# Kernel optimization log

Measured on AMD Instinct MI355X. Metric: run time of the kernel, lower is better.

## Reference

```python
import jax, jax.numpy as jnp
import numpy as np
import math

B, T, C, H, S_CACHE = 2, 1024, 2048, 16, 1024
DK = C // H


def setup_inputs() -> dict:
    key = jax.random.key(0)
    ks = jax.random.split(key, 7)
    x = jax.random.normal(ks[0], (B, T, C), dtype=jnp.float32)
    cache_k = jax.random.normal(ks[1], (B, H, S_CACHE, DK), dtype=jnp.float32)
    cache_v = jax.random.normal(ks[2], (B, H, S_CACHE, DK), dtype=jnp.float32)
    scale = 0.02
    Wq = jax.random.normal(ks[3], (C, C), dtype=jnp.float32) * scale
    Wk = jax.random.normal(ks[4], (C, C), dtype=jnp.float32) * scale
    Wv = jax.random.normal(ks[5], (C, C), dtype=jnp.float32) * scale
    Wo = jax.random.normal(ks[6], (C, C), dtype=jnp.float32) * scale
    return {"x": x, "cache_k": cache_k, "cache_v": cache_v,
            "Wq": Wq, "Wk": Wk, "Wv": Wv, "Wo": Wo}


def reference(x, cache_k, cache_v, Wq, Wk, Wv, Wo):
    b, t, c = x.shape
    h = cache_k.shape[1]
    dk = c // h
    # nn.Linear: y = x @ W.T  (weights stored [out, in])
    Q = (x @ Wq.T).reshape(b, t, h, dk).transpose(0, 2, 1, 3)  # [B,H,T,dk]
    K = (x @ Wk.T).reshape(b, t, h, dk).transpose(0, 2, 1, 3)
    V = (x @ Wv.T).reshape(b, t, h, dk).transpose(0, 2, 1, 3)
    K = jnp.concatenate([cache_k, K], axis=2)  # [B,H,S,dk]
    V = jnp.concatenate([cache_v, V], axis=2)
    s = K.shape[2]
    scores = jnp.einsum('bhtd,bhsd->bhts', Q, K) / math.sqrt(dk)
    # faithful to the source: mask = tril(ones(T, S)) (no cache offset); T==1 -> all ones
    if t == 1:
        mask = jnp.ones((1, s), dtype=jnp.float32)
    else:
        mask = jnp.tril(jnp.ones((t, s), dtype=jnp.float32))
    scores = jnp.where(mask == 0, jnp.float32(-jnp.inf), scores)
    attn = jax.nn.softmax(scores, axis=-1)
    out = jnp.einsum('bhts,bhsd->bhtd', attn, V)
    out = out.transpose(0, 2, 1, 3).reshape(b, t, c)
    return (out @ Wo.T, K, V)
```

## Files before the change

### kernel.cpp

```cpp
#include <hip/hip_runtime.h>

typedef unsigned short u16;
typedef short bf16x8 __attribute__((ext_vector_type(8)));
typedef float f32x4 __attribute__((ext_vector_type(4)));
typedef unsigned short u16x4 __attribute__((ext_vector_type(4)));

#define AS1 __attribute__((address_space(1)))
#define AS3 __attribute__((address_space(3)))

__device__ __forceinline__ u16 f2bf(float f) {
    unsigned u = __float_as_uint(f);
    u += 0x7fff + ((u >> 16) & 1);
    return (u16)(u >> 16);
}

__device__ __forceinline__ void gld16(const void* g, void* l) {
    __builtin_amdgcn_global_load_lds((const AS1 void*)g, (AS3 void*)l, 16, 0, 0);
}

__global__ void convall_kernel(const float* __restrict__ x,  const float* __restrict__ wq,
                               const float* __restrict__ wk, const float* __restrict__ wv,
                               const float* __restrict__ wo,
                               u16* __restrict__ xb, u16* __restrict__ wqkv, u16* __restrict__ wob) {
    int t = blockIdx.x * 256 + threadIdx.x;
    const float* srcs[5] = { x, wq, wk, wv, wo };
    u16* dsts[5] = { xb, wqkv, wqkv + 4194304, wqkv + 8388608, wob };
#pragma unroll
    for (int r = 0; r < 5; r++) {
        f32x4 v = ((const f32x4*)srcs[r])[t];
        u16x4 o = { f2bf(v.x), f2bf(v.y), f2bf(v.z), f2bf(v.w) };
        ((u16x4*)dsts[r])[t] = o;
    }
}

__global__ void cachek_kernel(const float* __restrict__ ck, float* __restrict__ kout,
                              u16* __restrict__ kcb) {
    const int n4 = (2 * 16 * 1024 * 128) / 4;
    int i = blockIdx.x * 256 + threadIdx.x;
    int stride = gridDim.x * 256;
    for (; i < n4; i += stride) {
        f32x4 v = ((const f32x4*)ck)[i];
        int bh = i >> 15;
        ((f32x4*)kout)[i + bh * 32768] = v;
        u16x4 o = { f2bf(v.x), f2bf(v.y), f2bf(v.z), f2bf(v.w) };
        ((u16x4*)kcb)[i] = o;
    }
}

__global__ void vtrans_kernel(const float* __restrict__ cv, float* __restrict__ vout,
                              u16* __restrict__ vtb) {
    __shared__ u16 tile[64 * 65];
    const int bh = blockIdx.x;
    const int s0 = blockIdx.y * 64;
    const int d0 = blockIdx.z * 64;
    const float* src = cv + (size_t)bh * 1024 * 128;
#pragma unroll
    for (int i = 0; i < 16; i++) {
        int e = i * 256 + threadIdx.x;
        int sr = e >> 6, dc = e & 63;
        float v = src[(size_t)(s0 + sr) * 128 + d0 + dc];
        vout[((size_t)bh * 2048 + s0 + sr) * 128 + d0 + dc] = v;
        tile[sr * 65 + dc] = f2bf(v);
    }
    __syncthreads();
    u16* dst = vtb + (size_t)bh * 128 * 1024;
#pragma unroll
    for (int i = 0; i < 16; i++) {
        int e = i * 256 + threadIdx.x;
        int dr = e >> 6, sc = e & 63;
        dst[(size_t)(d0 + dr) * 1024 + s0 + sc] = tile[sc * 65 + dr];
    }
}

template <int MODE>
__global__ __launch_bounds__(256) void gemm_bt_kernel(
    const u16* __restrict__ A, const u16* __restrict__ Bm,
    u16* __restrict__ qout, float* __restrict__ kout, float* __restrict__ vout,
    float* __restrict__ cout) {
    __shared__ u16 As[128 * 64];
    __shared__ u16 Bs[128 * 64];
    const int tid = threadIdx.x;
    const int lane = tid & 63, wv = tid >> 6;
    const int wm = (wv >> 1) * 64, wn = (wv & 1) * 64;
    const int m0 = blockIdx.y * 128, n0 = blockIdx.x * 128;
    const int frow = lane & 15, fq = lane >> 4;
    const int swz = frow & 7;

    f32x4 acc[4][4];
#pragma unroll
    for (int a = 0; a < 4; a++)
#pragma unroll
        for (int b = 0; b < 4; b++) acc[a][b] = (f32x4){0.f, 0.f, 0.f, 0.f};

    for (int k0 = 0; k0 < 2048; k0 += 64) {
        __syncthreads();
#pragma unroll
        for (int i = 0; i < 4; i++) {
            int L = i * 256 + tid;
            int row = L >> 3;
            int c = (L & 7) ^ (row & 7);
            gld16(A + (size_t)(m0 + row) * 2048 + k0 + c * 8, As + i * 2048 + wv * 512);
            gld16(Bm + (size_t)(n0 + row) * 2048 + k0 + c * 8, Bs + i * 2048 + wv * 512);
        }
        __syncthreads();
#pragma unroll
        for (int kk = 0; kk < 2; kk++) {
            bf16x8 aF[4], bF[4];
#pragma unroll
            for (int f = 0; f < 4; f++) {
                aF[f] = *(const bf16x8*)(As + (wm + f * 16 + frow) * 64 + ((kk * 4 + fq) ^ swz) * 8);
                bF[f] = *(const bf16x8*)(Bs + (wn + f * 16 + frow) * 64 + ((kk * 4 + fq) ^ swz) * 8);
            }
#pragma unroll
            for (int fm = 0; fm < 4; fm++)
#pragma unroll
                for (int fn = 0; fn < 4; fn++)
                    acc[fm][fn] = __builtin_amdgcn_mfma_f32_16x16x32_bf16(aF[fm], bF[fn], acc[fm][fn], 0, 0, 0);
        }
    }

#pragma unroll
    for (int fm = 0; fm < 4; fm++) {
#pragma unroll
        for (int fn = 0; fn < 4; fn++) {
#pragma unroll
            for (int r = 0; r < 4; r++) {
                int m = m0 + wm + fm * 16 + fq * 4 + r;
                int n = n0 + wn + fn * 16 + frow;
                float v = acc[fm][fn][r];
                if (MODE == 0) {
                    int b = m >> 10, t = m & 1023;
                    int sect = n >> 11, nn = n & 2047;
                    int h = nn >> 7, d = nn & 127;
                    size_t bh = (size_t)(b * 16 + h);
                    if (sect == 0)
                        qout[(bh * 1024 + t) * 128 + d] = f2bf(v * 0.08838834764831843f);
                    else if (sect == 1)
                        kout[(bh * 2048 + 1024 + t) * 128 + d] = v;
                    else
                        vout[(bh * 2048 + 1024 + t) * 128 + d] = v;
                } else {
                    cout[(size_t)m * 2048 + n] = v;
                }
            }
        }
    }
}

__global__ __launch_bounds__(256) void attn_kernel(
    const u16* __restrict__ Qb, const u16* __restrict__ Kcb,
    const u16* __restrict__ Vtb, u16* __restrict__ AOb) {
    __shared__ u16 Qs[64 * 128];
    __shared__ u16 Ks[64 * 128];
    __shared__ u16 Vs[128 * 64];
    __shared__ u16 Ps[64 * 64];
    int bid = blockIdx.x;
    int bh, qi;
    if (bid < 256) { bh = bid >> 4; qi = bid & 15; }
    else { int j = bid - 256; bh = 16 + (j >> 4); qi = 15 - (j & 15); }
    const int t0 = qi * 64;
    const int tid = threadIdx.x, lane = tid & 63, wv = tid >> 6;
    const int row_w = wv * 16;
    const int frow = lane & 15, fq = lane >> 4;
    const int swz = frow & 7;

    const u16* Qg = Qb + ((size_t)bh * 1024 + t0) * 128;
#pragma unroll
    for (int i = 0; i < 4; i++) {
        int L = i * 256 + tid;
        int row = L >> 4;
        int c = (L & 15) ^ (row & 7);
        gld16(Qg + row * 128 + c * 8, Qs + i * 2048 + wv * 512);
    }

    float mrow[4], lrow[4];
    f32x4 Oacc[8];
#pragma unroll
    for (int r = 0; r < 4; r++) { mrow[r] = -1e30f; lrow[r] = 0.f; }
#pragma unroll
    for (int fd = 0; fd < 8; fd++) Oacc[fd] = (f32x4){0.f, 0.f, 0.f, 0.f};

    const int nst = qi + 1;
    for (int st = 0; st < nst; st++) {
        int s0 = st * 64;
        __syncthreads();
        const u16* Kg = Kcb + ((size_t)bh * 1024 + s0) * 128;
#pragma unroll
        for (int i = 0; i < 4; i++) {
            int L = i * 256 + tid;
            int row = L >> 4;
            int c = (L & 15) ^ (row & 7);
            gld16(Kg + row * 128 + c * 8, Ks + i * 2048 + wv * 512);
        }
        const u16* Vg = Vtb + (size_t)bh * 131072 + s0;
#pragma unroll
        for (int i = 0; i < 4; i++) {
            int L = i * 256 + tid;
            int row = L >> 3;
            int c = (L & 7) ^ (row & 7);
            gld16(Vg + row * 1024 + c * 8, Vs + i * 2048 + wv * 512);
        }
        __syncthreads();

        f32x4 S[4];
#pragma unroll
        for (int fn = 0; fn < 4; fn++) S[fn] = (f32x4){0.f, 0.f, 0.f, 0.f};
#pragma unroll
        for (int kk = 0; kk < 4; kk++) {
            bf16x8 aF = *(const bf16x8*)(Qs + (row_w + frow) * 128 + ((kk * 4 + fq) ^ swz) * 8);
#pragma unroll
            for (int fn = 0; fn < 4; fn++) {
                bf16x8 bF = *(const bf16x8*)(Ks + (fn * 16 + frow) * 128 + ((kk * 4 + fq) ^ swz) * 8);
                S[fn] = __builtin_amdgcn_mfma_f32_16x16x32_bf16(aF, bF, S[fn], 0, 0, 0);
            }
        }

        if (st == qi) {
#pragma unroll
            for (int fn = 0; fn < 4; fn++)
#pragma unroll
                for (int r = 0; r < 4; r++) {
                    int t = t0 + row_w + fq * 4 + r;
                    int s = s0 + fn * 16 + frow;
                    if (s > t) S[fn][r] = -1e30f;
                }
        }

#pragma unroll
        for (int r = 0; r < 4; r++) {
            float mx = fmaxf(fmaxf(S[0][r], S[1][r]), fmaxf(S[2][r], S[3][r]));
            mx = fmaxf(mx, __shfl_xor(mx, 1));
            mx = fmaxf(mx, __shfl_xor(mx, 2));
            mx = fmaxf(mx, __shfl_xor(mx, 4));
            mx = fmaxf(mx, __shfl_xor(mx, 8));
            float mnew = fmaxf(mrow[r], mx);
            float alpha = __expf(mrow[r] - mnew);
            float rs = 0.f;
#pragma unroll
            for (int fn = 0; fn < 4; fn++) {
                float p = __expf(S[fn][r] - mnew);
                S[fn][r] = p;
                rs += p;
            }
            rs += __shfl_xor(rs, 1);
            rs += __shfl_xor(rs, 2);
            rs += __shfl_xor(rs, 4);
            rs += __shfl_xor(rs, 8);
            mrow[r] = mnew;
            lrow[r] = lrow[r] * alpha + rs;
#pragma unroll
            for (int fd = 0; fd < 8; fd++) Oacc[fd][r] *= alpha;
        }

#pragma unroll
        for (int fn = 0; fn < 4; fn++)
#pragma unroll
            for (int r = 0; r < 4; r++) {
                int pr = row_w + fq * 4 + r;
                int c = fn * 2 + (frow >> 3);
                Ps[pr * 64 + ((c ^ (pr & 7)) * 8) + (frow & 7)] = f2bf(S[fn][r]);
            }

#pragma unroll
        for (int ks = 0; ks < 2; ks++) {
            int rr = row_w + frow;
            bf16x8 aP = *(const bf16x8*)(Ps + rr * 64 + ((ks * 4 + fq) ^ (rr & 7)) * 8);
#pragma unroll
            for (int fd = 0; fd < 8; fd++) {
                int vr = fd * 16 + frow;
                bf16x8 bV = *(const bf16x8*)(Vs + vr * 64 + ((ks * 4 + fq) ^ (vr & 7)) * 8);
                Oacc[fd] = __builtin_amdgcn_mfma_f32_16x16x32_bf16(aP, bV, Oacc[fd], 0, 0, 0);
            }
        }
    }

    const int b = bh >> 4, h = bh & 15;
#pragma unroll
    for (int r = 0; r < 4; r++) {
        float rl = 1.0f / lrow[r];
        int t = t0 + row_w + fq * 4 + r;
#pragma unroll
        for (int fd = 0; fd < 8; fd++) {
            int col = h * 128 + fd * 16 + frow;
            AOb[((size_t)b * 1024 + t) * 2048 + col] = f2bf(Oacc[fd][r] * rl);
        }
    }
}

extern "C" void kernel_launch(void* const* d_in, const int* in_sizes, int n_in,
                              void* d_out, int out_size, void* d_ws, size_t ws_size,
                              hipStream_t stream) {
    const float* x  = (const float*)d_in[0];
    const float* ck = (const float*)d_in[1];
    const float* cv = (const float*)d_in[2];
    const float* Wq = (const float*)d_in[3];
    const float* Wk = (const float*)d_in[4];
    const float* Wv = (const float*)d_in[5];
    const float* Wo = (const float*)d_in[6];

    float* out  = (float*)d_out;
    float* Kout = out + 4194304;
    float* Vout = out + 12582912;

    u16* xb   = (u16*)d_ws;
    u16* Wqkv = xb + 4194304;
    u16* Wob  = Wqkv + 12582912;
    u16* Qb   = Wob + 4194304;
    u16* Kcb  = Qb + 4194304;
    u16* Vtb  = Kcb + 4194304;
    u16* AOb  = Vtb + 4194304;

    convall_kernel<<<4096, 256, 0, stream>>>(x, Wq, Wk, Wv, Wo, xb, Wqkv, Wob);
    cachek_kernel<<<1024, 256, 0, stream>>>(ck, Kout, Kcb);
    vtrans_kernel<<<dim3(32, 16, 2), 256, 0, stream>>>(cv, Vout, Vtb);

    gemm_bt_kernel<0><<<dim3(48, 16), 256, 0, stream>>>(xb, Wqkv, Qb, Kout, Vout, nullptr);
    attn_kernel<<<512, 256, 0, stream>>>(Qb, Kcb, Vtb, AOb);
    gemm_bt_kernel<1><<<dim3(16, 16), 256, 0, stream>>>(AOb, Wob, nullptr, nullptr, nullptr, out);
}
```

Measured before the change: 351.4 us.

## Split long causal attention rows across two blocks and shrink GEMM M-tile

For query tiles 8-15, the KV loop is split into two halves handled by separate blocks (flash-decoding style). Each block writes unnormalized partial outputs plus row max and sum to workspace reused from the Wqkv buffer, and a new merge kernel combines them into AOb. This is meant to balance the causal workload and raise block count on the attention launch. Separately, both GEMMs move from 128x128 to 64x128 tiles to double the grid and improve CU occupancy, at the cost of less data reuse per block, an extra launch, and a float32 partial round-trip through memory.

```diff
diff --git a/kernel.cpp b/kernel.cpp
--- a/kernel.cpp
+++ b/kernel.cpp
@@ -77,44 +77,51 @@
     const u16* __restrict__ A, const u16* __restrict__ Bm,
     u16* __restrict__ qout, float* __restrict__ kout, float* __restrict__ vout,
     float* __restrict__ cout) {
-    __shared__ u16 As[128 * 64];
+    __shared__ u16 As[64 * 64];
     __shared__ u16 Bs[128 * 64];
     const int tid = threadIdx.x;
     const int lane = tid & 63, wv = tid >> 6;
-    const int wm = (wv >> 1) * 64, wn = (wv & 1) * 64;
-    const int m0 = blockIdx.y * 128, n0 = blockIdx.x * 128;
+    const int wn = wv * 32;
+    const int m0 = blockIdx.y * 64, n0 = blockIdx.x * 128;
     const int frow = lane & 15, fq = lane >> 4;
     const int swz = frow & 7;
 
-    f32x4 acc[4][4];
+    f32x4 acc[4][2];
 #pragma unroll
     for (int a = 0; a < 4; a++)
 #pragma unroll
-        for (int b = 0; b < 4; b++) acc[a][b] = (f32x4){0.f, 0.f, 0.f, 0.f};
+        for (int b = 0; b < 2; b++) acc[a][b] = (f32x4){0.f, 0.f, 0.f, 0.f};
 
     for (int k0 = 0; k0 < 2048; k0 += 64) {
         __syncthreads();
+#pragma unroll
+        for (int i = 0; i < 2; i++) {
+            int L = i * 256 + tid;
+            int row = L >> 3;
+            int c = (L & 7) ^ (row & 7);
+            gld16(A + (size_t)(m0 + row) * 2048 + k0 + c * 8, As + i * 2048 + wv * 512);
+        }
 #pragma unroll
         for (int i = 0; i < 4; i++) {
             int L = i * 256 + tid;
             int row = L >> 3;
             int c = (L & 7) ^ (row & 7);
-            gld16(A + (size_t)(m0 + row) * 2048 + k0 + c * 8, As + i * 2048 + wv * 512);
             gld16(Bm + (size_t)(n0 + row) * 2048 + k0 + c * 8, Bs + i * 2048 + wv * 512);
         }
         __syncthreads();
 #pragma unroll
         for (int kk = 0; kk < 2; kk++) {
-            bf16x8 aF[4], bF[4];
-#pragma unroll
-            for (int f = 0; f < 4; f++) {
-                aF[f] = *(const bf16x8*)(As + (wm + f * 16 + frow) * 64 + ((kk * 4 + fq) ^ swz) * 8);
+            bf16x8 aF[4], bF[2];
+#pragma unroll
+            for (int f = 0; f < 4; f++)
+                aF[f] = *(const bf16x8*)(As + (f * 16 + frow) * 64 + ((kk * 4 + fq) ^ swz) * 8);
+#pragma unroll
+            for (int f = 0; f < 2; f++)
                 bF[f] = *(const bf16x8*)(Bs + (wn + f * 16 + frow) * 64 + ((kk * 4 + fq) ^ swz) * 8);
-            }
 #pragma unroll
             for (int fm = 0; fm < 4; fm++)
 #pragma unroll
-                for (int fn = 0; fn < 4; fn++)
+                for (int fn = 0; fn < 2; fn++)
                     acc[fm][fn] = __builtin_amdgcn_mfma_f32_16x16x32_bf16(aF[fm], bF[fn], acc[fm][fn], 0, 0, 0);
         }
     }
@@ -122,10 +129,10 @@
 #pragma unroll
     for (int fm = 0; fm < 4; fm++) {
 #pragma unroll
-        for (int fn = 0; fn < 4; fn++) {
+        for (int fn = 0; fn < 2; fn++) {
 #pragma unroll
             for (int r = 0; r < 4; r++) {
-                int m = m0 + wm + fm * 16 + fq * 4 + r;
+                int m = m0 + fm * 16 + fq * 4 + r;
                 int n = n0 + wn + fn * 16 + frow;
                 float v = acc[fm][fn][r];
                 if (MODE == 0) {
@@ -149,15 +156,32 @@
 
 __global__ __launch_bounds__(256) void attn_kernel(
     const u16* __restrict__ Qb, const u16* __restrict__ Kcb,
-    const u16* __restrict__ Vtb, u16* __restrict__ AOb) {
+    const u16* __restrict__ Vtb, u16* __restrict__ AOb,
+    float* __restrict__ PO, float* __restrict__ PML) {
     __shared__ u16 Qs[64 * 128];
     __shared__ u16 Ks[64 * 128];
     __shared__ u16 Vs[128 * 64];
     __shared__ u16 Ps[64 * 64];
-    int bid = blockIdx.x;
-    int bh, qi;
-    if (bid < 256) { bh = bid >> 4; qi = bid & 15; }
-    else { int j = bid - 256; bh = 16 + (j >> 4); qi = 15 - (j & 15); }
+    const int bid = blockIdx.x;
+    int bh, qi, st_begin, st_end, cidx;
+    bool partial;
+    if (bid < 512) {
+        qi = 15 - (bid >> 6);
+        int j = bid & 63;
+        bh = j >> 1;
+        int c = j & 1;
+        int n = qi + 1, h0 = (n + 1) >> 1;
+        st_begin = c ? h0 : 0;
+        st_end = c ? n : h0;
+        partial = true;
+        cidx = c * 256 + bh * 8 + (qi - 8);
+    } else {
+        int j = bid - 512;
+        qi = 7 - (j >> 5);
+        bh = j & 31;
+        st_begin = 0; st_end = qi + 1;
+        partial = false; cidx = 0;
+    }
     const int t0 = qi * 64;
     const int tid = threadIdx.x, lane = tid & 63, wv = tid >> 6;
     const int row_w = wv * 16;
@@ -180,8 +204,7 @@
 #pragma unroll
     for (int fd = 0; fd < 8; fd++) Oacc[fd] = (f32x4){0.f, 0.f, 0.f, 0.f};
 
-    const int nst = qi + 1;
-    for (int st = 0; st < nst; st++) {
+    for (int st = st_begin; st < st_end; st++) {
         int s0 = st * 64;
         __syncthreads();
         const u16* Kg = Kcb + ((size_t)bh * 1024 + s0) * 128;
@@ -274,16 +297,61 @@
         }
     }
 
+    if (partial) {
+        float* Od = PO + (size_t)cidx * 8192;
+#pragma unroll
+        for (int r = 0; r < 4; r++) {
+            int row = row_w + fq * 4 + r;
+#pragma unroll
+            for (int fd = 0; fd < 8; fd++)
+                Od[row * 128 + fd * 16 + frow] = Oacc[fd][r];
+        }
+        if (frow == 0) {
+#pragma unroll
+            for (int r = 0; r < 4; r++) {
+                int row = row_w + fq * 4 + r;
+                PML[cidx * 128 + row * 2] = mrow[r];
+                PML[cidx * 128 + row * 2 + 1] = lrow[r];
+            }
+        }
+    } else {
+        const int b = bh >> 4, h = bh & 15;
+#pragma unroll
+        for (int r = 0; r < 4; r++) {
+            float rl = 1.0f / lrow[r];
+            int t = t0 + row_w + fq * 4 + r;
+#pragma unroll
+            for (int fd = 0; fd < 8; fd++) {
+                int col = h * 128 + fd * 16 + frow;
+                AOb[((size_t)b * 1024 + t) * 2048 + col] = f2bf(Oacc[fd][r] * rl);
+            }
+        }
+    }
+}
+
+__global__ __launch_bounds__(256) void attn_merge_kernel(
+    const float* __restrict__ PO, const float* __restrict__ PML, u16* __restrict__ AOb) {
+    const int idx = blockIdx.x;
+    const int bh = idx >> 3, qi = 8 + (idx & 7);
+    const int t0 = qi * 64;
     const int b = bh >> 4, h = bh & 15;
-#pragma unroll
-    for (int r = 0; r < 4; r++) {
-        float rl = 1.0f / lrow[r];
-        int t = t0 + row_w + fq * 4 + r;
-#pragma unroll
-        for (int fd = 0; fd < 8; fd++) {
-            int col = h * 128 + fd * 16 + frow;
-            AOb[((size_t)b * 1024 + t) * 2048 + col] = f2bf(Oacc[fd][r] * rl);
-        }
+    const int tid = threadIdx.x;
+    const int row = tid >> 2, cg = tid & 3;
+    const float* O0 = PO + (size_t)idx * 8192;
+    const float* O1 = PO + (size_t)(256 + idx) * 8192;
+    float m0 = PML[idx * 128 + row * 2],        l0 = PML[idx * 128 + row * 2 + 1];
+    float m1 = PML[(256 + idx) * 128 + row * 2], l1 = PML[(256 + idx) * 128 + row * 2 + 1];
+    float mm = fmaxf(m0, m1);
+    float w0 = __expf(m0 - mm), w1 = __expf(m1 - mm);
+    float inv = 1.0f / (l0 * w0 + l1 * w1);
+    u16* dst = AOb + ((size_t)b * 1024 + t0 + row) * 2048 + h * 128 + cg * 32;
+#pragma unroll
+    for (int j = 0; j < 8; j++) {
+        f32x4 a = *(const f32x4*)(O0 + row * 128 + cg * 32 + j * 4);
+        f32x4 c = *(const f32x4*)(O1 + row * 128 + cg * 32 + j * 4);
+        u16x4 o = { f2bf((a.x * w0 + c.x * w1) * inv), f2bf((a.y * w0 + c.y * w1) * inv),
+                    f2bf((a.z * w0 + c.z * w1) * inv), f2bf((a.w * w0 + c.w * w1) * inv) };
+        *(u16x4*)(dst + j * 4) = o;
     }
 }
 
@@ -309,12 +377,15 @@
     u16* Kcb  = Qb + 4194304;
     u16* Vtb  = Kcb + 4194304;
     u16* AOb  = Vtb + 4194304;
+    float* PO  = (float*)Wqkv;
+    float* PML = PO + 4194304;
 
     convall_kernel<<<4096, 256, 0, stream>>>(x, Wq, Wk, Wv, Wo, xb, Wqkv, Wob);
     cachek_kernel<<<1024, 256, 0, stream>>>(ck, Kout, Kcb);
     vtrans_kernel<<<dim3(32, 16, 2), 256, 0, stream>>>(cv, Vout, Vtb);
 
-    gemm_bt_kernel<0><<<dim3(48, 16), 256, 0, stream>>>(xb, Wqkv, Qb, Kout, Vout, nullptr);
-    attn_kernel<<<512, 256, 0, stream>>>(Qb, Kcb, Vtb, AOb);
-    gemm_bt_kernel<1><<<dim3(16, 16), 256, 0, stream>>>(AOb, Wob, nullptr, nullptr, nullptr, out);
-}
+    gemm_bt_kernel<0><<<dim3(48, 32), 256, 0, stream>>>(xb, Wqkv, Qb, Kout, Vout, nullptr);
+    attn_kernel<<<768, 256, 0, stream>>>(Qb, Kcb, Vtb, AOb, PO, PML);
+    attn_merge_kernel<<<256, 256, 0, stream>>>(PO, PML, AOb);
+    gemm_bt_kernel<1><<<dim3(16, 32), 256, 0, stream>>>(AOb, Wob, nullptr, nullptr, nullptr, out);
+}
```

Result: faster. 324.8 us (-7.6%).
